# Kernel tuning notes

Measured on AMD Instinct MI355X. Metric: run time of the kernel, lower is better.

## Reference

```python
import jax, jax.numpy as jnp
import numpy as np

LOCAL_K = 3
TOKEN_T, TOKEN_H, TOKEN_W = 8, 32, 32  # N = T*H*W = 8192
HIDDEN, N_HEADS = 256, 8


def _gather_neighbors(kv):
    # kv: [B, N, D2] -> [B, N, 27, D2] of 3x3x3 neighborhood (zero padded)
    B, N, D2 = kv.shape
    pad = LOCAL_K // 2
    x3d = kv.reshape(B, TOKEN_T, TOKEN_H, TOKEN_W, D2)
    x3d = jnp.pad(x3d, ((0, 0), (pad, pad), (pad, pad), (pad, pad), (0, 0)))
    slices = [
        x3d[:, dt:dt + TOKEN_T, dh:dh + TOKEN_H, dw:dw + TOKEN_W, :]
        for dt in range(LOCAL_K)
        for dh in range(LOCAL_K)
        for dw in range(LOCAL_K)
    ]
    nb = jnp.stack(slices, axis=4)  # [B, T, H, W, 27, D2]
    return nb.reshape(B, N, LOCAL_K ** 3, D2)


def setup_inputs() -> dict:
    key = jax.random.key(0)
    k1, k2, k3 = jax.random.split(key, 3)
    B, N, D = 2, TOKEN_T * TOKEN_H * TOKEN_W, HIDDEN
    x = jax.random.normal(k1, (B, N, D), dtype=jnp.float32)
    w_qkv = jax.random.normal(k2, (3 * D, D), dtype=jnp.float32) * (D ** -0.5)
    w_out = jax.random.normal(k3, (D, D), dtype=jnp.float32) * (D ** -0.5)
    return {"x": x, "w_qkv": w_qkv, "w_out": w_out}


def reference(x, w_qkv, w_out):
    B, N, D = x.shape
    H, d = N_HEADS, D // N_HEADS
    qkv = x @ w_qkv.T                       # [B, N, 3D]
    q, k, v = jnp.split(qkv, 3, axis=-1)
    kv_nb = _gather_neighbors(jnp.concatenate([k, v], axis=-1))  # [B,N,27,2D]
    k_nb, v_nb = jnp.split(kv_nb, 2, axis=-1)
    q = q.reshape(B, N, H, d)
    k_nb = k_nb.reshape(B, N, 27, H, d)
    v_nb = v_nb.reshape(B, N, 27, H, d)
    scale = 1.0 / jnp.sqrt(jnp.asarray(d, dtype=q.dtype))
    scores = jnp.einsum('bnhd,bnkhd->bnhk', q, k_nb) * scale  # [B,N,H,27]
    attn = jax.nn.softmax(scores, axis=-1)
    out = jnp.einsum('bnhk,bnkhd->bnhd', attn, v_nb)           # [B,N,H,d]
    return out.reshape(B, N, D) @ w_out.T
```

## Files before the change

### kernel.cpp

```cpp
#include <hip/hip_runtime.h>
#include <hip/hip_bf16.h>

#define TOK_T 8
#define TOK_H 32
#define TOK_W 32
#define NTOK 8192
#define BATCH 2
#define DMODEL 256
#define D3 768
#define NHEADS 8
#define DHEAD 32

using short8  = __attribute__((ext_vector_type(8))) short;
using ushort8 = __attribute__((ext_vector_type(8))) unsigned short;
using f32x4   = __attribute__((ext_vector_type(4))) float;

__device__ __forceinline__ ushort f2bf(float f) {
  union { float f; unsigned u; } v; v.f = f;
  unsigned u = v.u;
  unsigned r = (u + 0x7FFFu + ((u >> 16) & 1u)) >> 16;
  return (ushort)r;
}
__device__ __forceinline__ float bf2f(ushort u) {
  union { unsigned u; float f; } v; v.u = ((unsigned)u) << 16;
  return v.f;
}

#define NX4  (BATCH * NTOK * DMODEL / 4)
#define NW14 (D3 * DMODEL / 4)
#define NW24 (DMODEL * DMODEL / 4)

__global__ __launch_bounds__(256) void convert_all(const float* __restrict__ x,
                                                   const float* __restrict__ wq,
                                                   const float* __restrict__ wo,
                                                   ushort* __restrict__ xb,
                                                   ushort* __restrict__ wqb,
                                                   ushort* __restrict__ wob) {
  int i = blockIdx.x * 256 + threadIdx.x;
  const float* src; ushort* dst; int j;
  if (i < NX4)              { src = x;  dst = xb;  j = i; }
  else if (i < NX4 + NW14)  { src = wq; dst = wqb; j = i - NX4; }
  else if (i < NX4 + NW14 + NW24) { src = wo; dst = wob; j = i - NX4 - NW14; }
  else return;
  float4 v = ((const float4*)src)[j];
  ushort4 o;
  o.x = f2bf(v.x); o.y = f2bf(v.y); o.z = f2bf(v.z); o.w = f2bf(v.w);
  ((ushort4*)dst)[j] = o;
}

#define BKK 32

template<int TBM, int TBN, int NW, bool OUT_BF16>
__global__ __launch_bounds__(NW * 64) void gemm_bt(const ushort* __restrict__ A,
                                                   const ushort* __restrict__ B,
                                                   void* __restrict__ Cv,
                                                   int M, int N, int K) {
  __shared__ __align__(16) ushort sA[2][TBM * BKK];
  __shared__ __align__(16) ushort sB[2][TBN * BKK];
  constexpr int NCW = TBN / 64;
  constexpr int CHA = TBM * 4;
  constexpr int CHB = TBN * 4;
  constexpr int CH  = CHA + CHB;
  constexpr int NT  = NW * 64;

  const int tid  = threadIdx.x;
  const int lane = tid & 63;
  const int wid  = tid >> 6;
  const int wr   = wid / NCW;
  const int wc   = wid % NCW;
  const int bm   = blockIdx.x * TBM;
  const int bn   = blockIdx.y * TBN;
  const int fr   = lane & 15;
  const int kb   = lane >> 4;

  f32x4 acc[4][4] = {};

  auto stage = [&](int buf, int kt) {
#pragma unroll
    for (int c0 = 0; c0 < CH; c0 += NT) {
      int c  = c0 + tid;
      int cb = c - lane;
      bool isA = (c < CHA);
      int cc  = isA ? c  : c - CHA;
      int cbb = isA ? cb : cb - CHA;
      int r  = cc >> 2;
      int sl = cc & 3;
      int ss = sl ^ ((r >> 1) & 3);
      const ushort* src = (isA ? A + (size_t)(bm + r) * K
                               : B + (size_t)(bn + r) * K) + kt + ss * 8;
      ushort* dst = isA ? &sA[buf][cbb * 8] : &sB[buf][cbb * 8];
      __builtin_amdgcn_global_load_lds((const __attribute__((address_space(1))) void*)src,
                                       (__attribute__((address_space(3))) void*)dst, 16, 0, 0);
    }
  };

  const int nit = K >> 5;
  stage(0, 0);
  __syncthreads();

  for (int it = 0; it < nit; ++it) {
    const int cur = it & 1;
    if (it + 1 < nit) stage(cur ^ 1, (it + 1) << 5);

    short8 af[4], bfr[4];
#pragma unroll
    for (int m = 0; m < 4; ++m) {
      int r  = wr * 64 + m * 16 + fr;
      int ck = r * 4 + (kb ^ ((r >> 1) & 3));
      af[m] = *(const short8*)&sA[cur][ck * 8];
    }
#pragma unroll
    for (int n = 0; n < 4; ++n) {
      int r  = wc * 64 + n * 16 + fr;
      int ck = r * 4 + (kb ^ ((r >> 1) & 3));
      bfr[n] = *(const short8*)&sB[cur][ck * 8];
    }
#pragma unroll
    for (int m = 0; m < 4; ++m)
#pragma unroll
      for (int n = 0; n < 4; ++n)
        acc[m][n] = __builtin_amdgcn_mfma_f32_16x16x32_bf16(af[m], bfr[n], acc[m][n], 0, 0, 0);
    __syncthreads();
  }

  if constexpr (OUT_BF16) {
    ushort* C = (ushort*)Cv;
#pragma unroll
    for (int m = 0; m < 4; ++m)
#pragma unroll
      for (int n = 0; n < 4; ++n)
#pragma unroll
        for (int j = 0; j < 4; ++j) {
          int row = bm + wr * 64 + m * 16 + kb * 4 + j;
          int col = bn + wc * 64 + n * 16 + fr;
          C[(size_t)row * N + col] = f2bf(acc[m][n][j]);
        }
  } else {
    float* C = (float*)Cv;
#pragma unroll
    for (int m = 0; m < 4; ++m)
#pragma unroll
      for (int n = 0; n < 4; ++n)
#pragma unroll
        for (int j = 0; j < 4; ++j) {
          int row = bm + wr * 64 + m * 16 + kb * 4 + j;
          int col = bn + wc * 64 + n * 16 + fr;
          C[(size_t)row * N + col] = acc[m][n][j];
        }
  }
}

#define TT 4
#define TLH 8
#define TLW 8
#define NHALO 600
#define KP 40

__global__ __launch_bounds__(256) void local_attn(const ushort* __restrict__ qkv,
                                                  ushort* __restrict__ aob) {
  __shared__ __align__(16) ushort sh[NHALO * KP];
  const int tile = blockIdx.x;
  const int head = blockIdx.y;
  const int b    = blockIdx.z;
  const int tz = tile >> 4;
  const int ty = (tile >> 2) & 3;
  const int tx = tile & 3;
  const int t0 = tz * TT, h0 = ty * TLH, w0 = tx * TLW;
  const int tid = threadIdx.x;

  auto stage = [&](int ofs) {
    for (int idx = tid; idx < NHALO; idx += 256) {
      int ht  = idx / 100;
      int rem = idx - ht * 100;
      int hh  = rem / 10;
      int hw  = rem - hh * 10;
      int gt = t0 - 1 + ht, gh = h0 - 1 + hh, gw = w0 - 1 + hw;
      ushort8* dst = (ushort8*)&sh[idx * KP];
      if (gt >= 0 && gt < TOK_T && gh >= 0 && gh < TOK_H && gw >= 0 && gw < TOK_W) {
        size_t base = ((size_t)b * NTOK + (size_t)gt * 1024 + gh * 32 + gw) * D3;
        const ushort8* s = (const ushort8*)(qkv + base + ofs + head * DHEAD);
#pragma unroll
        for (int p = 0; p < 4; ++p) dst[p] = s[p];
      } else {
        ushort8 z = (ushort8)0;
#pragma unroll
        for (int p = 0; p < 4; ++p) dst[p] = z;
      }
    }
  };

  stage(DMODEL);

  const int tt = tid >> 6;
  const int th = (tid >> 3) & 7;
  const int tw = tid & 7;
  const int n  = (t0 + tt) * 1024 + (h0 + th) * 32 + (w0 + tw);

  const ushort* qp = qkv + ((size_t)b * NTOK + n) * D3 + head * DHEAD;
  float q[DHEAD];
  {
    const ushort8* qs = (const ushort8*)qp;
#pragma unroll
    for (int p = 0; p < 4; ++p) {
      ushort8 v = qs[p];
#pragma unroll
      for (int e = 0; e < 8; ++e) q[p * 8 + e] = bf2f(v[e]);
    }
  }
  __syncthreads();

  const float scale = 0.1767766952966369f;
  float s[27];
#pragma unroll
  for (int nb = 0; nb < 27; ++nb) {
    int dt = nb / 9, dh = (nb / 3) % 3, dw = nb % 3;
    int hidx = (tt + dt) * 100 + (th + dh) * 10 + (tw + dw);
    const ushort8* kp = (const ushort8*)&sh[hidx * KP];
    float a = 0.f;
#pragma unroll
    for (int p = 0; p < 4; ++p) {
      ushort8 kk = kp[p];
#pragma unroll
      for (int e = 0; e < 8; ++e) a += q[p * 8 + e] * bf2f(kk[e]);
    }
    s[nb] = a * scale;
  }
  __syncthreads();

  stage(2 * DMODEL);

  float mx = s[0];
#pragma unroll
  for (int nb = 1; nb < 27; ++nb) mx = fmaxf(mx, s[nb]);
  __syncthreads();

  float o[DHEAD] = {};
  float sum = 0.f;
#pragma unroll
  for (int nb = 0; nb < 27; ++nb) {
    int dt = nb / 9, dh = (nb / 3) % 3, dw = nb % 3;
    int hidx = (tt + dt) * 100 + (th + dh) * 10 + (tw + dw);
    const ushort8* vp = (const ushort8*)&sh[hidx * KP];
    float p = __expf(s[nb] - mx);
    sum += p;
#pragma unroll
    for (int c = 0; c < 4; ++c) {
      ushort8 vv = vp[c];
#pragma unroll
      for (int e = 0; e < 8; ++e) o[c * 8 + e] += p * bf2f(vv[e]);
    }
  }

  float inv = 1.f / sum;
  ushort8 os[4];
#pragma unroll
  for (int c = 0; c < 4; ++c)
#pragma unroll
    for (int e = 0; e < 8; ++e) os[c][e] = f2bf(o[c * 8 + e] * inv);
  ushort8* op = (ushort8*)(aob + ((size_t)b * NTOK + n) * DMODEL + head * DHEAD);
#pragma unroll
  for (int c = 0; c < 4; ++c) op[c] = os[c];
}

extern "C" void kernel_launch(void* const* d_in, const int* in_sizes, int n_in,
                              void* d_out, int out_size, void* d_ws, size_t ws_size,
                              hipStream_t stream) {
  const float* x     = (const float*)d_in[0];
  const float* w_qkv = (const float*)d_in[1];
  const float* w_out = (const float*)d_in[2];
  float* out = (float*)d_out;

  char* ws = (char*)d_ws;
  size_t off = 0;
  ushort* xb    = (ushort*)(ws + off); off += (size_t)BATCH * NTOK * DMODEL * 2;
  ushort* wqkvb = (ushort*)(ws + off); off += (size_t)D3 * DMODEL * 2;
  ushort* woutb = (ushort*)(ws + off); off += (size_t)DMODEL * DMODEL * 2;
  ushort* qkvb  = (ushort*)(ws + off); off += (size_t)BATCH * NTOK * D3 * 2;
  ushort* aob   = (ushort*)(ws + off); off += (size_t)BATCH * NTOK * DMODEL * 2;

  int ntot = NX4 + NW14 + NW24;
  convert_all<<<(ntot + 255) / 256, 256, 0, stream>>>(x, w_qkv, w_out, xb, wqkvb, woutb);

  dim3 g1(BATCH * NTOK / 128, D3 / 256);
  gemm_bt<128, 256, 8, true><<<g1, 512, 0, stream>>>(xb, wqkvb, (void*)qkvb,
                                                     BATCH * NTOK, D3, DMODEL);

  dim3 ga(32, NHEADS, BATCH);
  local_attn<<<ga, 256, 0, stream>>>(qkvb, aob);

  dim3 g2(BATCH * NTOK / 64, DMODEL / 256);
  gemm_bt<64, 256, 4, false><<<g2, 256, 0, stream>>>(aob, woutb, (void*)out,
                                                     BATCH * NTOK, DMODEL, DMODEL);
}
```

Baseline: 67.50 us.

## Stage K and V halos together with swizzled LDS and packed bf16 math

The local attention kernel now loads the K and V halo for a tile into one XOR-swizzled shared buffer in a single pass. This removes the second staging phase and two block barriers. The dot products and value accumulation use two-wide float vectors with a packed bf16-pair unpack, which targets packed FMA instructions. The grid is flattened with a remapped block order, the GEMM grid axes are swapped so column tiles of the same rows run close together, launch bounds request two blocks per CU, and f2bf uses the library conversion. The larger shared buffer (about 77KB) may limit occupancy.

After: 59.62 us. 1.13x faster.

```diff
diff --git a/kernel.cpp b/kernel.cpp
--- a/kernel.cpp
+++ b/kernel.cpp
@@ -14,16 +14,22 @@
 using short8  = __attribute__((ext_vector_type(8))) short;
 using ushort8 = __attribute__((ext_vector_type(8))) unsigned short;
 using f32x4   = __attribute__((ext_vector_type(4))) float;
+using f32x2   = __attribute__((ext_vector_type(2))) float;
 
 __device__ __forceinline__ ushort f2bf(float f) {
-  union { float f; unsigned u; } v; v.f = f;
-  unsigned u = v.u;
-  unsigned r = (u + 0x7FFFu + ((u >> 16) & 1u)) >> 16;
-  return (ushort)r;
+  __hip_bfloat16 h = __float2bfloat16(f);
+  return *reinterpret_cast<ushort*>(&h);
 }
 __device__ __forceinline__ float bf2f(ushort u) {
   union { unsigned u; float f; } v; v.u = ((unsigned)u) << 16;
   return v.f;
+}
+__device__ __forceinline__ f32x2 bfpair(unsigned u) {
+  union { unsigned u; float f; } lo, hi;
+  lo.u = u << 16;
+  hi.u = u & 0xffff0000u;
+  f32x2 r; r[0] = lo.f; r[1] = hi.f;
+  return r;
 }
 
 #define NX4  (BATCH * NTOK * DMODEL / 4)
@@ -54,7 +60,7 @@
 __global__ __launch_bounds__(NW * 64) void gemm_bt(const ushort* __restrict__ A,
                                                    const ushort* __restrict__ B,
                                                    void* __restrict__ Cv,
-                                                   int M, int N, int K) {
+                                                   int N, int K) {
   __shared__ __align__(16) ushort sA[2][TBM * BKK];
   __shared__ __align__(16) ushort sB[2][TBN * BKK];
   constexpr int NCW = TBN / 64;
@@ -68,8 +74,8 @@
   const int wid  = tid >> 6;
   const int wr   = wid / NCW;
   const int wc   = wid % NCW;
-  const int bm   = blockIdx.x * TBM;
-  const int bn   = blockIdx.y * TBN;
+  const int bm   = blockIdx.y * TBM;
+  const int bn   = blockIdx.x * TBN;
   const int fr   = lane & 15;
   const int kb   = lane >> 4;
 
@@ -150,46 +156,41 @@
   }
 }
 
-#define TT 4
-#define TLH 8
-#define TLW 8
-#define NHALO 600
-#define KP 40
-
-__global__ __launch_bounds__(256) void local_attn(const ushort* __restrict__ qkv,
-                                                  ushort* __restrict__ aob) {
-  __shared__ __align__(16) ushort sh[NHALO * KP];
-  const int tile = blockIdx.x;
-  const int head = blockIdx.y;
-  const int b    = blockIdx.z;
-  const int tz = tile >> 4;
-  const int ty = (tile >> 2) & 3;
-  const int tx = tile & 3;
-  const int t0 = tz * TT, h0 = ty * TLH, w0 = tx * TLW;
+#define HALO 600
+
+__global__ __launch_bounds__(256, 2) void local_attn(const ushort* __restrict__ qkv,
+                                                     ushort* __restrict__ aob) {
+  __shared__ __align__(16) ushort sh[HALO * 64];
+  const int bid  = blockIdx.x;
+  const int grp  = bid & 7;
+  const int slot = bid >> 3;
+  const int tz = grp >> 2, ty = grp & 3;
+  const int tx   = slot & 3;
+  const int head = (slot >> 2) & 7;
+  const int b    = slot >> 5;
+  const int t0 = tz * 4, h0 = ty * 8, w0 = tx * 8;
   const int tid = threadIdx.x;
 
-  auto stage = [&](int ofs) {
-    for (int idx = tid; idx < NHALO; idx += 256) {
-      int ht  = idx / 100;
-      int rem = idx - ht * 100;
+#pragma unroll
+  for (int k = 0; k < 19; ++k) {
+    int u = tid + k * 256;
+    if (u < HALO * 8) {
+      int row = u >> 3;
+      int q   = u & 7;
+      int ht  = row / 100;
+      int rem = row - ht * 100;
       int hh  = rem / 10;
       int hw  = rem - hh * 10;
       int gt = t0 - 1 + ht, gh = h0 - 1 + hh, gw = w0 - 1 + hw;
-      ushort8* dst = (ushort8*)&sh[idx * KP];
+      uint4 v = {0u, 0u, 0u, 0u};
       if (gt >= 0 && gt < TOK_T && gh >= 0 && gh < TOK_H && gw >= 0 && gw < TOK_W) {
-        size_t base = ((size_t)b * NTOK + (size_t)gt * 1024 + gh * 32 + gw) * D3;
-        const ushort8* s = (const ushort8*)(qkv + base + ofs + head * DHEAD);
-#pragma unroll
-        for (int p = 0; p < 4; ++p) dst[p] = s[p];
-      } else {
-        ushort8 z = (ushort8)0;
-#pragma unroll
-        for (int p = 0; p < 4; ++p) dst[p] = z;
+        size_t base = ((size_t)b * NTOK + (size_t)gt * 1024 + gh * 32 + gw) * D3
+                      + head * DHEAD + (q < 4 ? DMODEL + q * 8 : 2 * DMODEL + (q - 4) * 8);
+        v = *(const uint4*)(qkv + base);
       }
-    }
-  };
-
-  stage(DMODEL);
+      *(uint4*)&sh[row * 64 + ((q ^ (row & 7)) * 8)] = v;
+    }
+  }
 
   const int tt = tid >> 6;
   const int th = (tid >> 3) & 7;
@@ -197,14 +198,16 @@
   const int n  = (t0 + tt) * 1024 + (h0 + th) * 32 + (w0 + tw);
 
   const ushort* qp = qkv + ((size_t)b * NTOK + n) * D3 + head * DHEAD;
-  float q[DHEAD];
+  f32x2 q2[16];
   {
     const ushort8* qs = (const ushort8*)qp;
 #pragma unroll
     for (int p = 0; p < 4; ++p) {
-      ushort8 v = qs[p];
-#pragma unroll
-      for (int e = 0; e < 8; ++e) q[p * 8 + e] = bf2f(v[e]);
+      union { ushort8 s; uint4 u; } v; v.s = qs[p];
+      q2[p * 4 + 0] = bfpair(v.u.x);
+      q2[p * 4 + 1] = bfpair(v.u.y);
+      q2[p * 4 + 2] = bfpair(v.u.z);
+      q2[p * 4 + 3] = bfpair(v.u.w);
     }
   }
   __syncthreads();
@@ -215,39 +218,42 @@
   for (int nb = 0; nb < 27; ++nb) {
     int dt = nb / 9, dh = (nb / 3) % 3, dw = nb % 3;
     int hidx = (tt + dt) * 100 + (th + dh) * 10 + (tw + dw);
-    const ushort8* kp = (const ushort8*)&sh[hidx * KP];
-    float a = 0.f;
+    const ushort* row = &sh[hidx * 64];
+    const int sw = hidx & 7;
+    f32x2 a2 = {0.f, 0.f};
 #pragma unroll
     for (int p = 0; p < 4; ++p) {
-      ushort8 kk = kp[p];
-#pragma unroll
-      for (int e = 0; e < 8; ++e) a += q[p * 8 + e] * bf2f(kk[e]);
-    }
-    s[nb] = a * scale;
-  }
-  __syncthreads();
-
-  stage(2 * DMODEL);
+      union { ushort8 s; uint4 u; } kk; kk.s = *(const ushort8*)&row[(p ^ sw) * 8];
+      a2 += q2[p * 4 + 0] * bfpair(kk.u.x);
+      a2 += q2[p * 4 + 1] * bfpair(kk.u.y);
+      a2 += q2[p * 4 + 2] * bfpair(kk.u.z);
+      a2 += q2[p * 4 + 3] * bfpair(kk.u.w);
+    }
+    s[nb] = (a2[0] + a2[1]) * scale;
+  }
 
   float mx = s[0];
 #pragma unroll
   for (int nb = 1; nb < 27; ++nb) mx = fmaxf(mx, s[nb]);
-  __syncthreads();
-
-  float o[DHEAD] = {};
+
+  f32x2 o2[16] = {};
   float sum = 0.f;
 #pragma unroll
   for (int nb = 0; nb < 27; ++nb) {
     int dt = nb / 9, dh = (nb / 3) % 3, dw = nb % 3;
     int hidx = (tt + dt) * 100 + (th + dh) * 10 + (tw + dw);
-    const ushort8* vp = (const ushort8*)&sh[hidx * KP];
+    const ushort* row = &sh[hidx * 64];
+    const int sw = hidx & 7;
     float p = __expf(s[nb] - mx);
     sum += p;
+    f32x2 p2; p2[0] = p; p2[1] = p;
 #pragma unroll
     for (int c = 0; c < 4; ++c) {
-      ushort8 vv = vp[c];
-#pragma unroll
-      for (int e = 0; e < 8; ++e) o[c * 8 + e] += p * bf2f(vv[e]);
+      union { ushort8 s; uint4 u; } vv; vv.s = *(const ushort8*)&row[((4 + c) ^ sw) * 8];
+      o2[c * 4 + 0] += p2 * bfpair(vv.u.x);
+      o2[c * 4 + 1] += p2 * bfpair(vv.u.y);
+      o2[c * 4 + 2] += p2 * bfpair(vv.u.z);
+      o2[c * 4 + 3] += p2 * bfpair(vv.u.w);
     }
   }
 
@@ -256,7 +262,8 @@
 #pragma unroll
   for (int c = 0; c < 4; ++c)
 #pragma unroll
-    for (int e = 0; e < 8; ++e) os[c][e] = f2bf(o[c * 8 + e] * inv);
+    for (int e = 0; e < 8; ++e)
+      os[c][e] = f2bf(o2[c * 4 + (e >> 1)][e & 1] * inv);
   ushort8* op = (ushort8*)(aob + ((size_t)b * NTOK + n) * DMODEL + head * DHEAD);
 #pragma unroll
   for (int c = 0; c < 4; ++c) op[c] = os[c];
@@ -281,14 +288,11 @@
   int ntot = NX4 + NW14 + NW24;
   convert_all<<<(ntot + 255) / 256, 256, 0, stream>>>(x, w_qkv, w_out, xb, wqkvb, woutb);
 
-  dim3 g1(BATCH * NTOK / 128, D3 / 256);
-  gemm_bt<128, 256, 8, true><<<g1, 512, 0, stream>>>(xb, wqkvb, (void*)qkvb,
-                                                     BATCH * NTOK, D3, DMODEL);
-
-  dim3 ga(32, NHEADS, BATCH);
-  local_attn<<<ga, 256, 0, stream>>>(qkvb, aob);
-
-  dim3 g2(BATCH * NTOK / 64, DMODEL / 256);
-  gemm_bt<64, 256, 4, false><<<g2, 256, 0, stream>>>(aob, woutb, (void*)out,
-                                                     BATCH * NTOK, DMODEL, DMODEL);
-}
+  gemm_bt<128, 256, 8, true><<<dim3(3, 128), 512, 0, stream>>>(xb, wqkvb, (void*)qkvb,
+                                                               D3, DMODEL);
+
+  local_attn<<<512, 256, 0, stream>>>(qkvb, aob);
+
+  gemm_bt<64, 256, 4, false><<<dim3(1, 256), 256, 0, stream>>>(aob, woutb, (void*)out,
+                                                               DMODEL, DMODEL);
+}
```
